# Optimization experiments

Measured on AMD Instinct MI355X. Metric: run time of the kernel, lower is better.

Reference implementation:

```python
import jax, jax.numpy as jnp
import numpy as np

# ---- dimensions ----
N = 16384      # nodes
E = 131072     # edges (avg degree 8)
F = 128        # scalar channel width == s_dim
L = 9          # spherical-harmonic components (lmax=2)
R = 8          # radial basis size
DOUT = L * F   # post-product node width (1152)
K = 1024       # fixed number of master nodes (static stand-in for m>0.5)
HID = 64       # master-selection hidden dim
DA = 64        # virtual-attention head dim
LAMBDA_ATTN = 0.5
R_CUT = 5.0
EPS = 1e-9


def sh_l2(u):
    # real SH polynomials up to l=2 on unit vectors u[..., 3] -> [..., 9]
    x, y, z = u[..., 0], u[..., 1], u[..., 2]
    o = jnp.ones_like(x)
    return jnp.stack([o, x, y, z, x * y, y * z, 3.0 * z * z - 1.0, x * z, x * x - y * y], axis=-1)


def bessel(r):
    # Bessel radial basis; r [..., 1] -> [..., R]
    n = jnp.arange(1, R + 1, dtype=r.dtype)
    return jnp.sqrt(2.0 / R_CUT) * jnp.sin(n * jnp.pi * r / R_CUT) / jnp.maximum(r, EPS)


def setup_inputs() -> dict:
    key = jax.random.key(0)
    ks = jax.random.split(key, 18)
    s = lambda d: 1.0 / np.sqrt(d)
    return {
        'h': jax.random.normal(ks[0], (N, F), jnp.float32),
        'pos': 3.0 * jax.random.normal(ks[1], (N, 3), jnp.float32),
        'edge_sh': jax.random.normal(ks[2], (E, L), jnp.float32),
        'edge_feats': jax.random.uniform(ks[3], (E, R), jnp.float32),
        'W_node_l': s(F) * jax.random.normal(ks[4], (F, F), jnp.float32),
        'W_rad_l': s(R) * jax.random.normal(ks[5], (R, F), jnp.float32),
        'W_prod_l': s(L * F) * jax.random.normal(ks[6], (L, F, DOUT), jnp.float32),
        'ms_W1': s(F) * jax.random.normal(ks[7], (F, HID), jnp.float32),
        'ms_b1': jnp.zeros((HID,), jnp.float32),
        'ms_W2': s(HID) * jax.random.normal(ks[8], (HID, 1), jnp.float32),
        'ms_b2': jnp.zeros((1,), jnp.float32),
        'vg_Wq': s(F) * jax.random.normal(ks[9], (F, DA), jnp.float32),
        'vg_Wk': s(F) * jax.random.normal(ks[10], (F, DA), jnp.float32),
        'W_node_h': s(DOUT) * jax.random.normal(ks[11], (DOUT, F), jnp.float32),
        'W_rad_h': s(R) * jax.random.normal(ks[12], (R, F), jnp.float32),
        'W_prod_h': s(L * F) * jax.random.normal(ks[13], (L, F, DOUT), jnp.float32),
        'edge_index': jax.random.randint(ks[14], (2, E), 0, N),
    }


def reference(h, pos, edge_sh, edge_feats, W_node_l, W_rad_l, W_prod_l,
              ms_W1, ms_b1, ms_W2, ms_b2, vg_Wq, vg_Wk,
              W_node_h, W_rad_h, W_prod_h, edge_index):
    src, dst = edge_index[0], edge_index[1]

    # ---- local conv + reshape + prod (with padded residual sc) ----
    t = (h[src] @ W_node_l) * (edge_feats @ W_rad_l)                      # [E,F]
    msg = edge_sh[:, :, None] * t[:, None, :]                             # [E,L,F]
    upd = jax.ops.segment_sum(msg, dst, num_segments=N)                   # [N,L,F]
    sc = jnp.pad(h, ((0, 0), (0, DOUT - F)))
    h_local = jnp.einsum('nlf,lfg->ng', upd, W_prod_l) + sc               # [N,DOUT]

    # ---- master selection (MLP -> sigmoid); fixed top-K masters ----
    hs = h_local[:, :F]
    m = jax.nn.sigmoid(jax.nn.relu(hs @ ms_W1 + ms_b1) @ ms_W2 + ms_b2)[:, 0]  # [N]
    _, midx = jax.lax.top_k(m, K)
    master_idx = jnp.sort(midx)                                           # [K]

    # ---- induced subgraph among masters as dense [K,K] adjacency ----
    rank = jnp.full((N,), K, dtype=jnp.int32).at[master_idx].set(jnp.arange(K, dtype=jnp.int32))
    adj = jnp.zeros((K + 1, K + 1), h.dtype).at[rank[src], rank[dst]].max(jnp.ones((E,), h.dtype))
    adj_induced = adj[:K, :K]

    h_m = h_local[master_idx]                                             # [K,DOUT]
    pos_m = pos[master_idx]                                               # [K,3]
    hms = h_m[:, :F]

    # ---- virtual graph generation (attention -> thresholded dense adj) ----
    q = hms @ vg_Wq
    kk = hms @ vg_Wk
    A = jax.nn.sigmoid(q @ kk.T / jnp.sqrt(jnp.asarray(DA, h.dtype)))     # [K,K]
    A_virtual = jnp.where(A > LAMBDA_ATTN, A, 0.0)
    eye = jnp.eye(K, dtype=bool)
    Bv = (A_virtual > 0) & ~eye                                           # remove self loops
    Bv = Bv | Bv.T                                                        # to_undirected
    adj_master = jnp.clip(adj_induced + Bv.astype(h.dtype), 0.0, 1.0) * (1.0 - jnp.eye(K, dtype=h.dtype))

    # ---- hierarchical conv over dense master graph ----
    A_rec = adj_master.T                                                  # A_rec[i,j]=1: sender j -> receiver i
    V = pos_m[None, :, :] - pos_m[:, None, :]                             # vec = pos[src]-pos[dst]
    r = jnp.linalg.norm(V, axis=-1, keepdims=True)                        # [K,K,1]
    u = V / jnp.maximum(r, EPS)
    sh_m = sh_l2(u)                                                       # [K,K,L]
    rad = bessel(r)                                                       # [K,K,R]
    tm = (h_m @ W_node_h)[None, :, :] * (rad @ W_rad_h) * A_rec[:, :, None]  # [K,K,F]
    upd_m = jnp.einsum('ijl,ijf->ilf', sh_m, tm)                          # [K,L,F]
    h_hier = jnp.einsum('ilf,lfg->ig', upd_m, W_prod_h) + h_m             # sc_master pad is 0-width

    # ---- masked scatter blend ----
    h_exp = jnp.zeros_like(h_local).at[master_idx].set(h_hier)
    h_final = (1.0 - m[:, None]) * h_local + m[:, None] * h_exp
    return (h_final, A_virtual, m, master_idx)
```

## Files before the change

### kernel.cpp

```cpp
#include <hip/hip_runtime.h>
#include <hip/hip_bf16.h>
#include <stdint.h>

#define N_NODES 16384
#define E_EDGES 131072
#define F_DIM 128
#define L_DIM 9
#define R_DIM 8
#define DOUT_DIM 1152
#define K_SEL 1024
#define HID_DIM 64
#define DA_DIM 64

typedef unsigned short u16;
typedef __attribute__((ext_vector_type(8))) short bf16x8;
typedef __attribute__((ext_vector_type(4))) float f32x4;

static __device__ inline u16 f2bs(float x) {
  union { __hip_bfloat16 b; u16 s; } u;
  u.b = __float2bfloat16(x);
  return u.s;
}

#define GLDS16(gsrc, ldst) __builtin_amdgcn_global_load_lds( \
    (__attribute__((address_space(1))) void*)(void*)(gsrc),  \
    (__attribute__((address_space(3))) void*)(ldst), 16, 0, 0)

__global__ __launch_bounds__(256) void gemm_mfma(
    const float* __restrict__ A, const u16* __restrict__ Bt,
    float* __restrict__ C, int ldc, int M, int Nc, int Kc,
    const float* __restrict__ Add, int ldadd, int addW)
{
  __shared__ float Af[128 * 32];
  __shared__ u16  Bs[128 * 32];
  const int tid = threadIdx.x;
  const int wave = tid >> 6, lane = tid & 63;
  const int wm = wave >> 1, wn = wave & 1;
  const int l15 = lane & 15, quad = lane >> 4;
  const int bm = blockIdx.y * 128, bn = blockIdx.x * 128;

  f32x4 acc[4][4];
#pragma unroll
  for (int i = 0; i < 4; i++)
#pragma unroll
    for (int j = 0; j < 4; j++) acc[i][j] = (f32x4)(0.f);

  for (int k0 = 0; k0 < Kc; k0 += 32) {
    __syncthreads();
#pragma unroll
    for (int it = 0; it < 4; it++) {
      int c = it * 256 + tid;
      int row = c >> 3, op = c & 7;
      int oct = op ^ (row & 7);
      const float* g = A + (size_t)(bm + row) * Kc + k0 + oct * 4;
      GLDS16(g, &Af[c * 4]);
    }
#pragma unroll
    for (int it = 0; it < 2; it++) {
      int c = it * 256 + tid;
      int row = c >> 2, qp = c & 3;
      int q = qp ^ ((row >> 1) & 3);
      const u16* g = Bt + (size_t)(bn + row) * Kc + k0 + q * 8;
      GLDS16(g, &Bs[c * 8]);
    }
    __syncthreads();

    bf16x8 af[4], bfg[4];
#pragma unroll
    for (int mi = 0; mi < 4; mi++) {
      int m = wm * 64 + mi * 16 + l15;
      int o0 = (quad * 2) ^ (m & 7), o1 = (quad * 2 + 1) ^ (m & 7);
      float4 lo = *(const float4*)&Af[m * 32 + o0 * 4];
      float4 hi = *(const float4*)&Af[m * 32 + o1 * 4];
      bf16x8 r;
      r[0] = (short)f2bs(lo.x); r[1] = (short)f2bs(lo.y);
      r[2] = (short)f2bs(lo.z); r[3] = (short)f2bs(lo.w);
      r[4] = (short)f2bs(hi.x); r[5] = (short)f2bs(hi.y);
      r[6] = (short)f2bs(hi.z); r[7] = (short)f2bs(hi.w);
      af[mi] = r;
    }
#pragma unroll
    for (int ni = 0; ni < 4; ni++) {
      int n = wn * 64 + ni * 16 + l15;
      int q2 = quad ^ ((n >> 1) & 3);
      bfg[ni] = *(const bf16x8*)&Bs[n * 32 + q2 * 8];
    }
#pragma unroll
    for (int mi = 0; mi < 4; mi++)
#pragma unroll
      for (int ni = 0; ni < 4; ni++)
        acc[mi][ni] = __builtin_amdgcn_mfma_f32_16x16x32_bf16(af[mi], bfg[ni], acc[mi][ni], 0, 0, 0);
  }
#pragma unroll
  for (int mi = 0; mi < 4; mi++)
#pragma unroll
    for (int ni = 0; ni < 4; ni++)
#pragma unroll
      for (int r = 0; r < 4; r++) {
        int row = bm + wm * 64 + mi * 16 + quad * 4 + r;
        int col = bn + wn * 64 + ni * 16 + l15;
        float v = acc[mi][ni][r];
        if (Add != nullptr && col < addW) v += Add[(size_t)row * ldadd + col];
        C[(size_t)row * ldc + col] = v;
      }
}

__global__ __launch_bounds__(256) void gemm_mfma_b16(
    const u16* __restrict__ A, const u16* __restrict__ Bt,
    float* __restrict__ C, int ldc, int Kc, int nbx, int nwg,
    const float* __restrict__ Add, int ldadd, int addW)
{
  __shared__ u16 As[2][128 * 32];
  __shared__ u16 Bs[2][128 * 32];
  const int tid = threadIdx.x;
  const int wave = tid >> 6, lane = tid & 63;
  const int wm = wave >> 1, wn = wave & 1;
  const int l15 = lane & 15, quad = lane >> 4;
  const int lin = blockIdx.x;
  const int swz = (lin & 7) * (nwg >> 3) + (lin >> 3);
  const int bm = (swz / nbx) * 128, bn = (swz % nbx) * 128;

  const int c0 = tid,      r0 = c0 >> 2, q0 = (c0 & 3) ^ ((r0 >> 1) & 3);
  const int c1 = 256 + tid, r1 = c1 >> 2, q1 = (c1 & 3) ^ ((r1 >> 1) & 3);
  const u16* gA0 = A + (size_t)(bm + r0) * Kc + q0 * 8;
  const u16* gA1 = A + (size_t)(bm + r1) * Kc + q1 * 8;
  const u16* gB0 = Bt + (size_t)(bn + r0) * Kc + q0 * 8;
  const u16* gB1 = Bt + (size_t)(bn + r1) * Kc + q1 * 8;

  f32x4 acc[4][4];
#pragma unroll
  for (int i = 0; i < 4; i++)
#pragma unroll
    for (int j = 0; j < 4; j++) acc[i][j] = (f32x4)(0.f);

#define STAGE_AB(s, k0) do {                      \
    GLDS16(gA0 + (k0), &As[s][c0 * 8]);           \
    GLDS16(gA1 + (k0), &As[s][c1 * 8]);           \
    GLDS16(gB0 + (k0), &Bs[s][c0 * 8]);           \
    GLDS16(gB1 + (k0), &Bs[s][c1 * 8]);           \
  } while (0)
#define RAWBAR() do { __builtin_amdgcn_s_barrier(); \
    __builtin_amdgcn_sched_barrier(0); } while (0)

  STAGE_AB(0, 0);
  asm volatile("s_waitcnt vmcnt(0)" ::: "memory");
  RAWBAR();
  int cur = 0;
  const int nt = Kc / 32;
  for (int t = 0; t < nt; t++) {
    if (t + 1 < nt) {
      STAGE_AB(cur ^ 1, (t + 1) * 32);
      asm volatile("s_waitcnt vmcnt(4)" ::: "memory");
    } else {
      asm volatile("s_waitcnt vmcnt(0)" ::: "memory");
    }
    RAWBAR();
    bf16x8 af[4], bfg[4];
#pragma unroll
    for (int mi = 0; mi < 4; mi++) {
      int m = wm * 64 + mi * 16 + l15;
      af[mi] = *(const bf16x8*)&As[cur][m * 32 + (quad ^ ((m >> 1) & 3)) * 8];
    }
#pragma unroll
    for (int ni = 0; ni < 4; ni++) {
      int n = wn * 64 + ni * 16 + l15;
      bfg[ni] = *(const bf16x8*)&Bs[cur][n * 32 + (quad ^ ((n >> 1) & 3)) * 8];
    }
#pragma unroll
    for (int mi = 0; mi < 4; mi++)
#pragma unroll
      for (int ni = 0; ni < 4; ni++)
        acc[mi][ni] = __builtin_amdgcn_mfma_f32_16x16x32_bf16(af[mi], bfg[ni], acc[mi][ni], 0, 0, 0);
    RAWBAR();
    cur ^= 1;
  }
#undef STAGE_AB
#undef RAWBAR

#pragma unroll
  for (int mi = 0; mi < 4; mi++)
#pragma unroll
    for (int ni = 0; ni < 4; ni++)
#pragma unroll
      for (int r = 0; r < 4; r++) {
        int row = bm + wm * 64 + mi * 16 + quad * 4 + r;
        int col = bn + wn * 64 + ni * 16 + l15;
        float v = acc[mi][ni][r];
        if (Add != nullptr && col < addW) v += Add[(size_t)row * ldadd + col];
        C[(size_t)row * ldc + col] = v;
      }
}

__global__ __launch_bounds__(256) void transpose_bf16(
    const float* __restrict__ W, u16* __restrict__ Bt, int K, int N)
{
  __shared__ float t[32][33];
  const int n0 = blockIdx.x * 32, k0 = blockIdx.y * 32;
  const int tx = threadIdx.x & 31, ty = threadIdx.x >> 5;
  for (int r = ty; r < 32; r += 8) t[r][tx] = W[(size_t)(k0 + r) * N + n0 + tx];
  __syncthreads();
  for (int r = ty; r < 32; r += 8) Bt[(size_t)(n0 + r) * K + k0 + tx] = f2bs(t[tx][r]);
}

__global__ __launch_bounds__(256) void hs_gemm_kernel(
    const float* __restrict__ A,
    const float* __restrict__ B,
    float* __restrict__ psum)
{
  __shared__ float As[16][129];
  __shared__ float Bs[16][128];
  const int tid = threadIdx.x;
  const int tx = tid & 15, ty = tid >> 4;
  const int bm = blockIdx.x * 128;
  const int z = blockIdx.y;
  const int kb = z * (DOUT_DIM / 4);
  const int ke = kb + DOUT_DIM / 4;
  const int ac = tid & 15, ar0 = tid >> 4;
  const int bc = tid & 127, br0 = tid >> 7;
  float acc[8][8];
#pragma unroll
  for (int i = 0; i < 8; i++)
#pragma unroll
    for (int j = 0; j < 8; j++) acc[i][j] = 0.f;

  float ra[8], rb[8];
#define LOADREG(k0) do {                                                       \
    _Pragma("unroll")                                                          \
    for (int rr = 0; rr < 8; rr++)                                             \
      ra[rr] = A[(size_t)(bm + ar0 + rr * 16) * DOUT_DIM + (k0) + ac];         \
    _Pragma("unroll")                                                          \
    for (int rr = 0; rr < 8; rr++)                                             \
      rb[rr] = B[(size_t)((k0) + br0 + rr * 2) * DOUT_DIM + bc];               \
  } while (0)

  LOADREG(kb);
  for (int k0 = kb; k0 < ke; k0 += 16) {
#pragma unroll
    for (int rr = 0; rr < 8; rr++) As[ac][ar0 + rr * 16] = ra[rr];
#pragma unroll
    for (int rr = 0; rr < 8; rr++) Bs[br0 + rr * 2][bc] = rb[rr];
    __syncthreads();
    if (k0 + 16 < ke) LOADREG(k0 + 16);
#pragma unroll
    for (int kk = 0; kk < 16; kk++) {
      float a[8], b[8];
#pragma unroll
      for (int i = 0; i < 8; i++) a[i] = As[kk][ty * 8 + i];
#pragma unroll
      for (int j = 0; j < 8; j++) b[j] = Bs[kk][tx * 8 + j];
#pragma unroll
      for (int i = 0; i < 8; i++)
#pragma unroll
        for (int j = 0; j < 8; j++) acc[i][j] = fmaf(a[i], b[j], acc[i][j]);
    }
    __syncthreads();
  }
#undef LOADREG
#pragma unroll
  for (int i = 0; i < 8; i++) {
    size_t row = (size_t)z * N_NODES + bm + ty * 8 + i;
#pragma unroll
    for (int j = 0; j < 8; j++)
      psum[row * F_DIM + tx * 8 + j] = acc[i][j];
  }
}

__global__ __launch_bounds__(256) void hs_reduce_kernel(
    const float* __restrict__ psum, const float* __restrict__ h, float* __restrict__ hs)
{
  size_t i4 = (size_t)blockIdx.x * 256 + threadIdx.x;
  const size_t stride = (size_t)N_NODES * F_DIM / 4;
  const float4* p = (const float4*)psum;
  float4 a = p[i4], b = p[i4 + stride], c = p[i4 + 2 * stride], d = p[i4 + 3 * stride];
  float4 hh = ((const float4*)h)[i4];
  float4 o;
  o.x = a.x + b.x + c.x + d.x + hh.x;
  o.y = a.y + b.y + c.y + d.y + hh.y;
  o.z = a.z + b.z + c.z + d.z + hh.z;
  o.w = a.w + b.w + c.w + d.w + hh.w;
  ((float4*)hs)[i4] = o;
}

__global__ __launch_bounds__(256) void gemm64_f32(
    const float* __restrict__ A, int lda,
    const float* __restrict__ B, int ldb,
    float* __restrict__ C, int ldc,
    int M, int Nc, int Kc, int kPerSplit,
    const float* __restrict__ Add, int ldadd, int addW)
{
  __shared__ float As[16][65];
  __shared__ float Bs[16][64];
  const int tid = threadIdx.x;
  const int tx = tid & 15, ty = tid >> 4;
  const int bm = blockIdx.y * 64, bn = blockIdx.x * 64;
  const int kb = blockIdx.z * kPerSplit;
  const int ke = min(kb + kPerSplit, Kc);
  float acc[4][4];
#pragma unroll
  for (int i = 0; i < 4; i++)
#pragma unroll
    for (int j = 0; j < 4; j++) acc[i][j] = 0.f;
  for (int k0 = kb; k0 < ke; k0 += 16) {
    const int ac = tid & 15, ar = tid >> 4;
#pragma unroll
    for (int rr = 0; rr < 4; rr++) {
      int row = ar + rr * 16;
      As[ac][row] = A[(size_t)(bm + row) * lda + k0 + ac];
    }
    const int bc = tid & 63, br = tid >> 6;
#pragma unroll
    for (int rr = 0; rr < 4; rr++) {
      int kr = br + rr * 4;
      Bs[kr][bc] = B[(size_t)(k0 + kr) * ldb + bn + bc];
    }
    __syncthreads();
#pragma unroll
    for (int kk = 0; kk < 16; kk++) {
      float a[4], b[4];
#pragma unroll
      for (int i = 0; i < 4; i++) a[i] = As[kk][ty * 4 + i];
#pragma unroll
      for (int j = 0; j < 4; j++) b[j] = Bs[kk][tx * 4 + j];
#pragma unroll
      for (int i = 0; i < 4; i++)
#pragma unroll
        for (int j = 0; j < 4; j++) acc[i][j] = fmaf(a[i], b[j], acc[i][j]);
    }
    __syncthreads();
  }
#pragma unroll
  for (int i = 0; i < 4; i++) {
    int row = bm + ty * 4 + i;
#pragma unroll
    for (int j = 0; j < 4; j++) {
      int col = bn + tx * 4 + j;
      if (gridDim.z > 1) {
        atomicAdd(&C[(size_t)row * ldc + col], acc[i][j]);
      } else {
        float v = acc[i][j];
        if (Add != nullptr && col < addW) v += Add[(size_t)row * ldadd + col];
        C[(size_t)row * ldc + col] = v;
      }
    }
  }
}

__global__ __launch_bounds__(256) void count_kernel(
    const int* __restrict__ ei, int* __restrict__ counts)
{
  int e = blockIdx.x * 256 + threadIdx.x;
  atomicAdd(&counts[ei[E_EDGES + e]], 1);
}

__global__ __launch_bounds__(1024) void scan_kernel(
    const int* __restrict__ counts, int* __restrict__ offsets, int* __restrict__ cursor)
{
  __shared__ int part[1024];
  const int t = threadIdx.x;
  const int base = t * 16;
  int loc[16];
  int s = 0;
#pragma unroll
  for (int k = 0; k < 16; k++) { loc[k] = counts[base + k]; s += loc[k]; }
  part[t] = s;
  __syncthreads();
  for (int d = 1; d < 1024; d <<= 1) {
    int v = (t >= d) ? part[t - d] : 0;
    __syncthreads();
    part[t] += v;
    __syncthreads();
  }
  int run = part[t] - s;
#pragma unroll
  for (int k = 0; k < 16; k++) {
    offsets[base + k] = run;
    cursor[base + k] = run;
    run += loc[k];
  }
}

__global__ __launch_bounds__(256) void fill_kernel(
    const int* __restrict__ ei, int* __restrict__ cursor, int* __restrict__ elist)
{
  int e = blockIdx.x * 256 + threadIdx.x;
  int d = ei[E_EDGES + e];
  int p = atomicAdd(&cursor[d], 1);
  elist[p] = e;
}

__global__ __launch_bounds__(128) void gather_accum_kernel(
    const float* __restrict__ hW, const float* __restrict__ edge_sh,
    const float* __restrict__ edge_feats, const float* __restrict__ W_rad_l,
    const int* __restrict__ ei, const int* __restrict__ offsets,
    const int* __restrict__ counts, const int* __restrict__ elist,
    float* __restrict__ upd, u16* __restrict__ updb)
{
  const int d = blockIdx.x, f = threadIdx.x;
  const float w0 = W_rad_l[0 * F_DIM + f], w1 = W_rad_l[1 * F_DIM + f];
  const float w2 = W_rad_l[2 * F_DIM + f], w3 = W_rad_l[3 * F_DIM + f];
  const float w4 = W_rad_l[4 * F_DIM + f], w5 = W_rad_l[5 * F_DIM + f];
  const float w6 = W_rad_l[6 * F_DIM + f], w7 = W_rad_l[7 * F_DIM + f];
  const int b = offsets[d], n = counts[d];
  float acc[L_DIM];
#pragma unroll
  for (int l = 0; l < L_DIM; l++) acc[l] = 0.f;
  for (int k = 0; k < n; k++) {
    const int e = elist[b + k];
    const int s = ei[e];
    const float4 ef0 = *(const float4*)&edge_feats[(size_t)e * R_DIM];
    const float4 ef1 = *(const float4*)&edge_feats[(size_t)e * R_DIM + 4];
    float rw = ef0.x * w0;
    rw = fmaf(ef0.y, w1, rw); rw = fmaf(ef0.z, w2, rw); rw = fmaf(ef0.w, w3, rw);
    rw = fmaf(ef1.x, w4, rw); rw = fmaf(ef1.y, w5, rw);
    rw = fmaf(ef1.z, w6, rw); rw = fmaf(ef1.w, w7, rw);
    const float tf = hW[(size_t)s * F_DIM + f] * rw;
#pragma unroll
    for (int l = 0; l < L_DIM; l++)
      acc[l] = fmaf(edge_sh[(size_t)e * L_DIM + l], tf, acc[l]);
  }
#pragma unroll
  for (int l = 0; l < L_DIM; l++)
    upd[(size_t)d * DOUT_DIM + l * F_DIM + f] = acc[l];
  if (updb != nullptr) {
#pragma unroll
    for (int l = 0; l < L_DIM; l++)
      updb[(size_t)d * DOUT_DIM + l * F_DIM + f] = f2bs(acc[l]);
  }
}

__global__ __launch_bounds__(256) void gate_kernel(
    const float* __restrict__ hs, const float* __restrict__ W1,
    const float* __restrict__ b1, const float* __restrict__ W2,
    const float* __restrict__ b2, float* __restrict__ m_ws, float* __restrict__ m_out,
    int* __restrict__ hist1)
{
  __shared__ float sW1[F_DIM * HID_DIM];
  __shared__ float srow[4][F_DIM];
  const int tid = threadIdx.x;
  for (int t = tid; t < F_DIM * HID_DIM; t += 256) sW1[t] = W1[t];
  const int wave = tid >> 6, lane = tid & 63;
  const int n = blockIdx.x * 4 + wave;
  srow[wave][lane] = hs[(size_t)n * F_DIM + lane];
  srow[wave][lane + 64] = hs[(size_t)n * F_DIM + lane + 64];
  __syncthreads();
  float hid = b1[lane];
#pragma unroll 8
  for (int c = 0; c < F_DIM; c++) hid = fmaf(srow[wave][c], sW1[c * HID_DIM + lane], hid);
  hid = fmaxf(hid, 0.f);
  float v = hid * W2[lane];
#pragma unroll
  for (int off = 32; off > 0; off >>= 1) v += __shfl_down(v, off);
  if (lane == 0) {
    float mm = 1.f / (1.f + expf(-(v + b2[0])));
    m_ws[n] = mm;
    m_out[n] = mm;
    unsigned mb = __float_as_uint(mm);
    atomicAdd(&hist1[mb >> 16], 1);
  }
}

__global__ __launch_bounds__(1024) void radix_sel_kernel(
    const int* __restrict__ hist, const int* __restrict__ kin, int kinIdx,
    int* __restrict__ outp, int outIdx)
{
  __shared__ int part[1024];
  const int t = threadIdx.x;
  const int Kv = kin ? kin[kinIdx] : K_SEL;
  const int base = t * 64;
  int s = 0;
  for (int k = 0; k < 64; k++) s += hist[base + k];
  part[t] = s;
  __syncthreads();
  for (int d = 1; d < 1024; d <<= 1) {
    int v = (t + d < 1024) ? part[t + d] : 0;
    __syncthreads();
    part[t] += v;
    __syncthreads();
  }
  int inc = part[t];
  if (inc >= Kv && inc - s < Kv) {
    int r = inc - s;
    for (int b = base + 63; b >= base; b--) {
      int hv = hist[b];
      if (r + hv >= Kv) { outp[outIdx] = b; outp[outIdx + 1] = Kv - r; break; }
      r += hv;
    }
  }
}

__global__ __launch_bounds__(256) void hist2_kernel(
    const float* __restrict__ m_ws, const int* __restrict__ selb, int* __restrict__ hist2)
{
  int i = blockIdx.x * 256 + threadIdx.x;
  unsigned mb = __float_as_uint(m_ws[i]);
  if ((int)(mb >> 16) == selb[0]) atomicAdd(&hist2[mb & 0xFFFFu], 1);
}

__global__ __launch_bounds__(256) void flag_kernel(
    const float* __restrict__ m_ws, int* __restrict__ selb,
    unsigned char* __restrict__ flags, int* __restrict__ cand)
{
  int i = blockIdx.x * 256 + threadIdx.x;
  unsigned mb = __float_as_uint(m_ws[i]);
  unsigned vb = ((unsigned)selb[0] << 16) | (unsigned)selb[2];
  unsigned char fl = 0;
  if (mb > vb) fl = 1;
  else if (mb == vb) { int p = atomicAdd(&selb[4], 1); cand[p] = i; }
  flags[i] = fl;
}

__global__ __launch_bounds__(1024) void cand_kernel(
    const int* __restrict__ selb, const int* __restrict__ cand, unsigned char* __restrict__ flags)
{
  const int nc = selb[4], need = selb[3];
  for (int c = threadIdx.x; c < nc; c += 1024) {
    const int idx = cand[c];
    int r = 0;
    for (int o = 0; o < nc; o++) r += (cand[o] < idx) ? 1 : 0;
    if (r < need) flags[idx] = 1;
  }
}

__global__ __launch_bounds__(1024) void compact_kernel(
    const unsigned char* __restrict__ flags, int* __restrict__ midx,
    int* __restrict__ rank, float* __restrict__ mi_out)
{
  __shared__ int part[1024];
  const int t = threadIdx.x;
  const int base = t * 16;
  int loc[16];
  int s = 0;
#pragma unroll
  for (int k = 0; k < 16; k++) { loc[k] = flags[base + k]; s += loc[k]; }
  part[t] = s;
  __syncthreads();
  for (int d = 1; d < 1024; d <<= 1) {
    int v = (t >= d) ? part[t - d] : 0;
    __syncthreads();
    part[t] += v;
    __syncthreads();
  }
  int run = part[t] - s;
#pragma unroll
  for (int k = 0; k < 16; k++) {
    int i = base + k;
    if (loc[k]) {
      midx[run] = i;
      mi_out[run] = (float)i;
      rank[i] = run;
      run++;
    } else {
      rank[i] = K_SEL;
    }
  }
}

__global__ __launch_bounds__(256) void adj_kernel(
    const int* __restrict__ ei, const int* __restrict__ rank,
    unsigned char* __restrict__ adjm, unsigned char* __restrict__ adjT)
{
  int e = blockIdx.x * 256 + threadIdx.x;
  int rs = rank[ei[e]];
  int rd = rank[ei[E_EDGES + e]];
  if (rs < K_SEL && rd < K_SEL) {
    adjm[(size_t)rs * K_SEL + rd] = 1;
    adjT[(size_t)rd * K_SEL + rs] = 1;
  }
}

__global__ __launch_bounds__(128) void gather_kernel(
    const float* __restrict__ hl, const float* __restrict__ pos,
    const int* __restrict__ midx, float* __restrict__ h_m, float* __restrict__ pos_m)
{
  const int rI = blockIdx.x, t = threadIdx.x;
  const int mi = midx[rI];
  const float4* src = (const float4*)(hl + (size_t)mi * DOUT_DIM);
  float4* dst = (float4*)(h_m + (size_t)rI * DOUT_DIM);
  for (int c = t; c < DOUT_DIM / 4; c += 128) dst[c] = src[c];
  if (t < 3) pos_m[rI * 3 + t] = pos[mi * 3 + t];
}

__global__ __launch_bounds__(128) void qk_kernel(
    const float* __restrict__ hs, const int* __restrict__ midx,
    const float* __restrict__ Wq, const float* __restrict__ Wk,
    float* __restrict__ q, float* __restrict__ kk)
{
  __shared__ float row[F_DIM];
  const int i = blockIdx.x, t = threadIdx.x;
  const int mi = midx[i];
  row[t] = hs[(size_t)mi * F_DIM + t];
  __syncthreads();
  const int d = t & 63;
  const float* W = (t < 64) ? Wq : Wk;
  float acc = 0.f;
#pragma unroll 8
  for (int c = 0; c < F_DIM; c++) acc = fmaf(row[c], W[c * DA_DIM + d], acc);
  float* dst = (t < 64) ? q : kk;
  dst[(size_t)i * DA_DIM + d] = acc;
}

__global__ __launch_bounds__(256) void attn_kernel(
    const float* __restrict__ q, const float* __restrict__ kk,
    unsigned char* __restrict__ maskA, unsigned char* __restrict__ maskAT,
    float* __restrict__ Av)
{
  __shared__ float qs[16][DA_DIM + 1], ks[16][DA_DIM + 1];
  const int tx = threadIdx.x, ty = threadIdx.y;
  const int tid = ty * 16 + tx;
  const int i0 = blockIdx.y * 16, j0 = blockIdx.x * 16;
  for (int t = tid; t < 16 * DA_DIM; t += 256) {
    int rr = t >> 6, cc = t & 63;
    qs[rr][cc] = q[(size_t)(i0 + rr) * DA_DIM + cc];
    ks[rr][cc] = kk[(size_t)(j0 + rr) * DA_DIM + cc];
  }
  __syncthreads();
  float acc = 0.f;
#pragma unroll
  for (int d2 = 0; d2 < DA_DIM; d2++) acc = fmaf(qs[ty][d2], ks[tx][d2], acc);
  float sgl = 1.f / (1.f + expf(-acc * 0.125f));
  size_t o = (size_t)(i0 + ty) * K_SEL + (j0 + tx);
  bool big = sgl > 0.5f;
  unsigned char bb = big ? 1 : 0;
  maskA[o] = bb;
  maskAT[(size_t)(j0 + tx) * K_SEL + (i0 + ty)] = bb;
  Av[o] = big ? sgl : 0.f;
}

__global__ __launch_bounds__(256) void listbuild_kernel(
    const unsigned char* __restrict__ adjT, const unsigned char* __restrict__ maskAT,
    const unsigned char* __restrict__ maskA, u16* __restrict__ list, int* __restrict__ nj)
{
  __shared__ int cnt;
  const int i = blockIdx.x, tid = threadIdx.x;
  const int lane = tid & 63;
  if (tid == 0) cnt = 0;
  __syncthreads();
  const int j0 = tid * 4;
  uchar4 a  = *(const uchar4*)&adjT  [(size_t)i * K_SEL + j0];
  uchar4 mt = *(const uchar4*)&maskAT[(size_t)i * K_SEL + j0];
  uchar4 ma = *(const uchar4*)&maskA [(size_t)i * K_SEL + j0];
  unsigned char av[4];
  av[0] = a.x | mt.x | ma.x; av[1] = a.y | mt.y | ma.y;
  av[2] = a.z | mt.z | ma.z; av[3] = a.w | mt.w | ma.w;
#pragma unroll
  for (int r = 0; r < 4; r++) {
    int j = j0 + r;
    bool e = (j != i) && av[r];
    unsigned long long m = __ballot(e);
    int nset = __popcll(m);
    int base = 0;
    if (lane == 0 && nset) base = atomicAdd(&cnt, nset);
    base = __shfl(base, 0);
    if (e) {
      int p = base + __popcll(m & ((1ull << lane) - 1ull));
      list[(size_t)i * K_SEL + p] = (u16)j;
    }
  }
  __syncthreads();
  if (tid == 0) nj[i] = cnt;
}

__global__ __launch_bounds__(512) void hier2_kernel(
    const float* __restrict__ hWn, const float* __restrict__ pos_m,
    const float* __restrict__ W_rad_h, const u16* __restrict__ list,
    const int* __restrict__ nj, float* __restrict__ upd_m, u16* __restrict__ updb_m)
{
  __shared__ float gsm[128][20];
  __shared__ float red[3][L_DIM][F_DIM];
  const int tid = threadIdx.x;
  const int i = blockIdx.x;
  const int f = tid & 127, jsub = tid >> 7;
  const float sw0 = W_rad_h[0 * F_DIM + f], sw1 = W_rad_h[1 * F_DIM + f];
  const float sw2 = W_rad_h[2 * F_DIM + f], sw3 = W_rad_h[3 * F_DIM + f];
  const float sw4 = W_rad_h[4 * F_DIM + f], sw5 = W_rad_h[5 * F_DIM + f];
  const float sw6 = W_rad_h[6 * F_DIM + f], sw7 = W_rad_h[7 * F_DIM + f];
  const float pix = pos_m[i * 3 + 0], piy = pos_m[i * 3 + 1], piz = pos_m[i * 3 + 2];
  float acc[L_DIM];
#pragma unroll
  for (int l = 0; l < L_DIM; l++) acc[l] = 0.f;
  const int n = nj[i];
  for (int c0 = 0; c0 < n; c0 += 128) {
    const int cnt = min(128, n - c0);
    __syncthreads();
    if (tid < cnt) {
      const int j = list[(size_t)i * K_SEL + c0 + tid];
      float vx = pos_m[j * 3 + 0] - pix;
      float vy = pos_m[j * 3 + 1] - piy;
      float vz = pos_m[j * 3 + 2] - piz;
      float r = sqrtf(vx * vx + vy * vy + vz * vz);
      float rm = fmaxf(r, 1e-9f);
      float inv = 1.f / rm;
      float ux = vx * inv, uy = vy * inv, uz = vz * inv;
      float theta = 0.62831853071795864769f * r;
      float s1 = sinf(theta), c1 = cosf(theta);
      float coef = 0.632455532033675866f * inv;
      float snm2 = 0.f, snm1 = s1;
      gsm[tid][0] = s1 * coef;
#pragma unroll
      for (int nn = 2; nn <= R_DIM; nn++) {
        float sn = 2.f * c1 * snm1 - snm2;
        gsm[tid][nn - 1] = sn * coef;
        snm2 = snm1; snm1 = sn;
      }
      gsm[tid][8] = 1.f; gsm[tid][9] = ux; gsm[tid][10] = uy; gsm[tid][11] = uz;
      gsm[tid][12] = ux * uy; gsm[tid][13] = uy * uz;
      gsm[tid][14] = 3.f * uz * uz - 1.f;
      gsm[tid][15] = ux * uz; gsm[tid][16] = ux * ux - uy * uy;
      gsm[tid][17] = __int_as_float(j);
      gsm[tid][18] = 0.f; gsm[tid][19] = 0.f;
    }
    __syncthreads();
    for (int t = jsub; t < cnt; t += 4) {
      float2 s2 = *(const float2*)&gsm[t][16];
      const int j = __float_as_int(s2.y);
      const float hw = hWn[(size_t)j * F_DIM + f];
      float4 r0 = *(const float4*)&gsm[t][0];
      float4 r1 = *(const float4*)&gsm[t][4];
      float4 s0 = *(const float4*)&gsm[t][8];
      float4 s1g = *(const float4*)&gsm[t][12];
      float rw = r0.x * sw0;
      rw = fmaf(r0.y, sw1, rw); rw = fmaf(r0.z, sw2, rw); rw = fmaf(r0.w, sw3, rw);
      rw = fmaf(r1.x, sw4, rw); rw = fmaf(r1.y, sw5, rw);
      rw = fmaf(r1.z, sw6, rw); rw = fmaf(r1.w, sw7, rw);
      const float tm = hw * rw;
      acc[0] = fmaf(s0.x, tm, acc[0]); acc[1] = fmaf(s0.y, tm, acc[1]);
      acc[2] = fmaf(s0.z, tm, acc[2]); acc[3] = fmaf(s0.w, tm, acc[3]);
      acc[4] = fmaf(s1g.x, tm, acc[4]); acc[5] = fmaf(s1g.y, tm, acc[5]);
      acc[6] = fmaf(s1g.z, tm, acc[6]); acc[7] = fmaf(s1g.w, tm, acc[7]);
      acc[8] = fmaf(s2.x, tm, acc[8]);
    }
  }
  __syncthreads();
  if (jsub > 0) {
#pragma unroll
    for (int l = 0; l < L_DIM; l++) red[jsub - 1][l][f] = acc[l];
  }
  __syncthreads();
  if (jsub == 0) {
#pragma unroll
    for (int l = 0; l < L_DIM; l++) {
      float v = acc[l] + red[0][l][f] + red[1][l][f] + red[2][l][f];
      upd_m[(size_t)i * DOUT_DIM + l * F_DIM + f] = v;
      updb_m[(size_t)i * DOUT_DIM + l * F_DIM + f] = f2bs(v);
    }
  }
}

__global__ __launch_bounds__(256) void combine_kernel(
    float* __restrict__ out0, const float* __restrict__ h_hier,
    const float* __restrict__ m_ws, const int* __restrict__ rank)
{
  size_t i4 = (size_t)blockIdx.x * 256 + threadIdx.x;
  int n = (int)(i4 / (DOUT_DIM / 4));
  int g4 = (int)(i4 % (DOUT_DIM / 4));
  float mv = m_ws[n];
  int r = rank[n];
  float4 hl = ((const float4*)out0)[i4];
  float4 he = make_float4(0.f, 0.f, 0.f, 0.f);
  if (r < K_SEL) he = ((const float4*)h_hier)[(size_t)r * (DOUT_DIM / 4) + g4];
  float4 o;
  o.x = (1.f - mv) * hl.x + mv * he.x;
  o.y = (1.f - mv) * hl.y + mv * he.y;
  o.z = (1.f - mv) * hl.z + mv * he.z;
  o.w = (1.f - mv) * hl.w + mv * he.w;
  ((float4*)out0)[i4] = o;
}

extern "C" void kernel_launch(void* const* d_in, const int* in_sizes, int n_in,
                              void* d_out, int out_size, void* d_ws, size_t ws_size,
                              hipStream_t stream)
{
  const float* h         = (const float*)d_in[0];
  const float* pos       = (const float*)d_in[1];
  const float* edge_sh   = (const float*)d_in[2];
  const float* edge_feats= (const float*)d_in[3];
  const float* W_node_l  = (const float*)d_in[4];
  const float* W_rad_l   = (const float*)d_in[5];
  const float* W_prod_l  = (const float*)d_in[6];
  const float* ms_W1     = (const float*)d_in[7];
  const float* ms_b1     = (const float*)d_in[8];
  const float* ms_W2     = (const float*)d_in[9];
  const float* ms_b2     = (const float*)d_in[10];
  const float* vg_Wq     = (const float*)d_in[11];
  const float* vg_Wk     = (const float*)d_in[12];
  const float* W_node_h  = (const float*)d_in[13];
  const float* W_rad_h   = (const float*)d_in[14];
  const float* W_prod_h  = (const float*)d_in[15];
  const int*   eidx      = (const int*)d_in[16];

  float* out    = (float*)d_out;
  float* out_hf = out;
  float* out_Av = out + (size_t)N_NODES * DOUT_DIM;
  float* out_m  = out_Av + (size_t)K_SEL * K_SEL;
  float* out_mi = out_m + N_NODES;

  char* ws = (char*)d_ws;
  float* upd = (float*)ws;
  float* hW  = (float*)(ws + (size_t)N_NODES * DOUT_DIM * 4);
  float* hs  = hW;
  const size_t updbOff = (size_t)N_NODES * DOUT_DIM * 4 + (size_t)N_NODES * F_DIM * 4;
  const size_t updbNeed = updbOff + (size_t)N_NODES * DOUT_DIM * 2;
  const bool useB16 = (ws_size >= updbNeed);
  u16* updb = (u16*)(ws + updbOff);
  float* psum = out_hf;
  u16* Btl = (u16*)out_Av;
  char* csr = (char*)out_Av + (((size_t)DOUT_DIM * DOUT_DIM * 2 + 255) & ~(size_t)255);
  int* counts  = (int*)csr;
  int* offsets = counts + N_NODES;
  int* cursor  = offsets + N_NODES;
  int* elist   = cursor + N_NODES;
  size_t off = 0;
  auto alloc = [&](size_t bytes) -> void* {
    void* p = ws + off;
    off += (bytes + 255) & ~(size_t)255;
    return p;
  };
  float* m_ws  = (float*)alloc((size_t)N_NODES * 4);
  int*   rank  = (int*)alloc((size_t)N_NODES * 4);
  int*   midx  = (int*)alloc((size_t)K_SEL * 4);
  int*   hist1 = (int*)alloc((size_t)65536 * 4);
  int*   hist2 = (int*)alloc((size_t)65536 * 4);
  int*   selb  = (int*)alloc((size_t)64 * 4);
  int*   cand  = (int*)alloc((size_t)N_NODES * 4);
  unsigned char* flags = (unsigned char*)alloc((size_t)N_NODES);
  unsigned char* adjm  = (unsigned char*)alloc((size_t)K_SEL * K_SEL);
  unsigned char* adjT  = (unsigned char*)alloc((size_t)K_SEL * K_SEL);
  unsigned char* maskA = (unsigned char*)alloc((size_t)K_SEL * K_SEL);
  unsigned char* maskAT= (unsigned char*)alloc((size_t)K_SEL * K_SEL);
  float* qbuf  = (float*)alloc((size_t)K_SEL * DA_DIM * 4);
  float* kbuf  = (float*)alloc((size_t)K_SEL * DA_DIM * 4);
  float* h_m   = (float*)alloc((size_t)K_SEL * DOUT_DIM * 4);
  float* pos_m = (float*)alloc((size_t)K_SEL * 3 * 4);
  float* hWn   = (float*)alloc((size_t)K_SEL * F_DIM * 4);
  float* upd_m = (float*)alloc((size_t)K_SEL * DOUT_DIM * 4);
  float* h_hier= (float*)alloc((size_t)K_SEL * DOUT_DIM * 4);
  u16*   Bth   = (u16*)alloc((size_t)DOUT_DIM * DOUT_DIM * 2);
  u16*   jlist = (u16*)alloc((size_t)K_SEL * K_SEL * 2);
  int*   njbuf = (int*)alloc((size_t)K_SEL * 4);
  u16*   updbm = (u16*)alloc((size_t)K_SEL * DOUT_DIM * 2);

  hipMemsetAsync(counts, 0, (size_t)N_NODES * 4, stream);
  transpose_bf16<<<dim3(DOUT_DIM / 32, DOUT_DIM / 32), 256, 0, stream>>>(
      W_prod_l, Btl, DOUT_DIM, DOUT_DIM);
  gemm64_f32<<<dim3(F_DIM / 64, N_NODES / 64, 1), 256, 0, stream>>>(
      h, F_DIM, W_node_l, F_DIM, hW, F_DIM, N_NODES, F_DIM, F_DIM, F_DIM, nullptr, 0, 0);
  count_kernel<<<E_EDGES / 256, 256, 0, stream>>>(eidx, counts);
  scan_kernel<<<1, 1024, 0, stream>>>(counts, offsets, cursor);
  fill_kernel<<<E_EDGES / 256, 256, 0, stream>>>(eidx, cursor, elist);
  gather_accum_kernel<<<N_NODES, 128, 0, stream>>>(
      hW, edge_sh, edge_feats, W_rad_l, eidx, offsets, counts, elist, upd,
      useB16 ? updb : nullptr);
  hs_gemm_kernel<<<dim3(N_NODES / 128, 4), 256, 0, stream>>>(upd, W_prod_l, psum);
  hs_reduce_kernel<<<(N_NODES * F_DIM / 4) / 256, 256, 0, stream>>>(psum, h, hs);
  if (useB16) {
    gemm_mfma_b16<<<(DOUT_DIM / 128) * (N_NODES / 128), 256, 0, stream>>>(
        updb, Btl, out_hf, DOUT_DIM, DOUT_DIM, DOUT_DIM / 128,
        (DOUT_DIM / 128) * (N_NODES / 128), h, F_DIM, F_DIM);
  } else {
    gemm_mfma<<<dim3(DOUT_DIM / 128, N_NODES / 128), 256, 0, stream>>>(
        upd, Btl, out_hf, DOUT_DIM, N_NODES, DOUT_DIM, DOUT_DIM, h, F_DIM, F_DIM);
  }

  hipMemsetAsync(adjm, 0, (size_t)2 * K_SEL * K_SEL, stream);
  hipMemsetAsync(hist1, 0, (size_t)65536 * 4 * 2 + 256, stream);
  transpose_bf16<<<dim3(DOUT_DIM / 32, DOUT_DIM / 32), 256, 0, stream>>>(
      W_prod_h, Bth, DOUT_DIM, DOUT_DIM);
  gate_kernel<<<N_NODES / 4, 256, 0, stream>>>(hs, ms_W1, ms_b1, ms_W2, ms_b2,
                                               m_ws, out_m, hist1);
  radix_sel_kernel<<<1, 1024, 0, stream>>>(hist1, nullptr, 0, selb, 0);
  hist2_kernel<<<N_NODES / 256, 256, 0, stream>>>(m_ws, selb, hist2);
  radix_sel_kernel<<<1, 1024, 0, stream>>>(hist2, selb, 1, selb, 2);
  flag_kernel<<<N_NODES / 256, 256, 0, stream>>>(m_ws, selb, flags, cand);
  cand_kernel<<<1, 1024, 0, stream>>>(selb, cand, flags);
  compact_kernel<<<1, 1024, 0, stream>>>(flags, midx, rank, out_mi);
  adj_kernel<<<E_EDGES / 256, 256, 0, stream>>>(eidx, rank, adjm, adjT);
  gather_kernel<<<K_SEL, 128, 0, stream>>>(out_hf, pos, midx, h_m, pos_m);
  qk_kernel<<<K_SEL, 128, 0, stream>>>(hs, midx, vg_Wq, vg_Wk, qbuf, kbuf);
  attn_kernel<<<dim3(K_SEL / 16, K_SEL / 16), dim3(16, 16), 0, stream>>>(
      qbuf, kbuf, maskA, maskAT, out_Av);
  listbuild_kernel<<<K_SEL, 256, 0, stream>>>(adjT, maskAT, maskA, jlist, njbuf);
  hipMemsetAsync(hWn, 0, (size_t)K_SEL * F_DIM * 4, stream);
  gemm64_f32<<<dim3(F_DIM / 64, K_SEL / 64, 4), 256, 0, stream>>>(
      h_m, DOUT_DIM, W_node_h, F_DIM, hWn, F_DIM,
      K_SEL, F_DIM, DOUT_DIM, DOUT_DIM / 4, nullptr, 0, 0);
  hier2_kernel<<<K_SEL, 512, 0, stream>>>(hWn, pos_m, W_rad_h, jlist, njbuf, upd_m, updbm);
  gemm_mfma_b16<<<(DOUT_DIM / 128) * (K_SEL / 128), 256, 0, stream>>>(
      updbm, Bth, h_hier, DOUT_DIM, DOUT_DIM, DOUT_DIM / 128,
      (DOUT_DIM / 128) * (K_SEL / 128), h_m, DOUT_DIM, DOUT_DIM);
  combine_kernel<<<(N_NODES * DOUT_DIM / 4) / 256, 256, 0, stream>>>(out_hf, h_hier, m_ws, rank);
}
```

Measured before the change: 667.8 us.

## Fuse candidate tie-break into compaction, retile hier2 kernel, simplify GEMM barriers

Merges the candidate tie-break kernel into the compaction kernel, saving one single-block launch. The hier2 kernel is remapped to 256 threads that each handle two feature channels, and it no longer writes the unused fp32 upd_m buffer, only the bf16 copy. The bf16 MFMA GEMM drops its hand-placed vmcnt waits and scheduling barriers in favour of one __syncthreads per K step. This relies on __syncthreads also waiting for the async LDS loads. The barrier change can reduce load/compute overlap, and halving threads in hier2 lowers occupancy while raising per-thread work.

```diff
diff --git a/kernel.cpp b/kernel.cpp
--- a/kernel.cpp
+++ b/kernel.cpp
@@ -139,22 +139,13 @@
     GLDS16(gB0 + (k0), &Bs[s][c0 * 8]);           \
     GLDS16(gB1 + (k0), &Bs[s][c1 * 8]);           \
   } while (0)
-#define RAWBAR() do { __builtin_amdgcn_s_barrier(); \
-    __builtin_amdgcn_sched_barrier(0); } while (0)
 
   STAGE_AB(0, 0);
-  asm volatile("s_waitcnt vmcnt(0)" ::: "memory");
-  RAWBAR();
+  __syncthreads();
   int cur = 0;
   const int nt = Kc / 32;
   for (int t = 0; t < nt; t++) {
-    if (t + 1 < nt) {
-      STAGE_AB(cur ^ 1, (t + 1) * 32);
-      asm volatile("s_waitcnt vmcnt(4)" ::: "memory");
-    } else {
-      asm volatile("s_waitcnt vmcnt(0)" ::: "memory");
-    }
-    RAWBAR();
+    if (t + 1 < nt) STAGE_AB(cur ^ 1, (t + 1) * 32);
     bf16x8 af[4], bfg[4];
 #pragma unroll
     for (int mi = 0; mi < 4; mi++) {
@@ -171,11 +162,10 @@
 #pragma unroll
       for (int ni = 0; ni < 4; ni++)
         acc[mi][ni] = __builtin_amdgcn_mfma_f32_16x16x32_bf16(af[mi], bfg[ni], acc[mi][ni], 0, 0, 0);
-    RAWBAR();
+    __syncthreads();
     cur ^= 1;
   }
 #undef STAGE_AB
-#undef RAWBAR
 
 #pragma unroll
   for (int mi = 0; mi < 4; mi++)
@@ -509,24 +499,21 @@
   flags[i] = fl;
 }
 
-__global__ __launch_bounds__(1024) void cand_kernel(
-    const int* __restrict__ selb, const int* __restrict__ cand, unsigned char* __restrict__ flags)
-{
+__global__ __launch_bounds__(1024) void compact_kernel(
+    const int* __restrict__ selb, const int* __restrict__ cand,
+    unsigned char* flags, int* __restrict__ midx,
+    int* __restrict__ rank, float* __restrict__ mi_out)
+{
+  __shared__ int part[1024];
+  const int t = threadIdx.x;
   const int nc = selb[4], need = selb[3];
-  for (int c = threadIdx.x; c < nc; c += 1024) {
+  for (int c = t; c < nc; c += 1024) {
     const int idx = cand[c];
     int r = 0;
     for (int o = 0; o < nc; o++) r += (cand[o] < idx) ? 1 : 0;
     if (r < need) flags[idx] = 1;
   }
-}
-
-__global__ __launch_bounds__(1024) void compact_kernel(
-    const unsigned char* __restrict__ flags, int* __restrict__ midx,
-    int* __restrict__ rank, float* __restrict__ mi_out)
-{
-  __shared__ int part[1024];
-  const int t = threadIdx.x;
+  __syncthreads();
   const int base = t * 16;
   int loc[16];
   int s = 0;
@@ -660,24 +647,29 @@
   if (tid == 0) nj[i] = cnt;
 }
 
-__global__ __launch_bounds__(512) void hier2_kernel(
+__global__ __launch_bounds__(256) void hier2_kernel(
     const float* __restrict__ hWn, const float* __restrict__ pos_m,
     const float* __restrict__ W_rad_h, const u16* __restrict__ list,
-    const int* __restrict__ nj, float* __restrict__ upd_m, u16* __restrict__ updb_m)
+    const int* __restrict__ nj, u16* __restrict__ updb_m)
 {
   __shared__ float gsm[128][20];
   __shared__ float red[3][L_DIM][F_DIM];
   const int tid = threadIdx.x;
   const int i = blockIdx.x;
-  const int f = tid & 127, jsub = tid >> 7;
-  const float sw0 = W_rad_h[0 * F_DIM + f], sw1 = W_rad_h[1 * F_DIM + f];
-  const float sw2 = W_rad_h[2 * F_DIM + f], sw3 = W_rad_h[3 * F_DIM + f];
-  const float sw4 = W_rad_h[4 * F_DIM + f], sw5 = W_rad_h[5 * F_DIM + f];
-  const float sw6 = W_rad_h[6 * F_DIM + f], sw7 = W_rad_h[7 * F_DIM + f];
+  const int lane = tid & 63, jsub = tid >> 6;
+  const int f0 = lane, f1 = lane + 64;
+  const float a0 = W_rad_h[0 * F_DIM + f0], a1 = W_rad_h[1 * F_DIM + f0];
+  const float a2 = W_rad_h[2 * F_DIM + f0], a3 = W_rad_h[3 * F_DIM + f0];
+  const float a4 = W_rad_h[4 * F_DIM + f0], a5 = W_rad_h[5 * F_DIM + f0];
+  const float a6 = W_rad_h[6 * F_DIM + f0], a7 = W_rad_h[7 * F_DIM + f0];
+  const float b0 = W_rad_h[0 * F_DIM + f1], b1 = W_rad_h[1 * F_DIM + f1];
+  const float b2 = W_rad_h[2 * F_DIM + f1], b3 = W_rad_h[3 * F_DIM + f1];
+  const float b4 = W_rad_h[4 * F_DIM + f1], b5 = W_rad_h[5 * F_DIM + f1];
+  const float b6 = W_rad_h[6 * F_DIM + f1], b7 = W_rad_h[7 * F_DIM + f1];
   const float pix = pos_m[i * 3 + 0], piy = pos_m[i * 3 + 1], piz = pos_m[i * 3 + 2];
-  float acc[L_DIM];
-#pragma unroll
-  for (int l = 0; l < L_DIM; l++) acc[l] = 0.f;
+  float acc0[L_DIM], acc1[L_DIM];
+#pragma unroll
+  for (int l = 0; l < L_DIM; l++) { acc0[l] = 0.f; acc1[l] = 0.f; }
   const int n = nj[i];
   for (int c0 = 0; c0 < n; c0 += 128) {
     const int cnt = min(128, n - c0);
@@ -713,35 +705,49 @@
     for (int t = jsub; t < cnt; t += 4) {
       float2 s2 = *(const float2*)&gsm[t][16];
       const int j = __float_as_int(s2.y);
-      const float hw = hWn[(size_t)j * F_DIM + f];
+      const float hw0 = hWn[(size_t)j * F_DIM + f0];
+      const float hw1 = hWn[(size_t)j * F_DIM + f1];
       float4 r0 = *(const float4*)&gsm[t][0];
       float4 r1 = *(const float4*)&gsm[t][4];
       float4 s0 = *(const float4*)&gsm[t][8];
       float4 s1g = *(const float4*)&gsm[t][12];
-      float rw = r0.x * sw0;
-      rw = fmaf(r0.y, sw1, rw); rw = fmaf(r0.z, sw2, rw); rw = fmaf(r0.w, sw3, rw);
-      rw = fmaf(r1.x, sw4, rw); rw = fmaf(r1.y, sw5, rw);
-      rw = fmaf(r1.z, sw6, rw); rw = fmaf(r1.w, sw7, rw);
-      const float tm = hw * rw;
-      acc[0] = fmaf(s0.x, tm, acc[0]); acc[1] = fmaf(s0.y, tm, acc[1]);
-      acc[2] = fmaf(s0.z, tm, acc[2]); acc[3] = fmaf(s0.w, tm, acc[3]);
-      acc[4] = fmaf(s1g.x, tm, acc[4]); acc[5] = fmaf(s1g.y, tm, acc[5]);
-      acc[6] = fmaf(s1g.z, tm, acc[6]); acc[7] = fmaf(s1g.w, tm, acc[7]);
-      acc[8] = fmaf(s2.x, tm, acc[8]);
+      float rwa = r0.x * a0;
+      rwa = fmaf(r0.y, a1, rwa); rwa = fmaf(r0.z, a2, rwa); rwa = fmaf(r0.w, a3, rwa);
+      rwa = fmaf(r1.x, a4, rwa); rwa = fmaf(r1.y, a5, rwa);
+      rwa = fmaf(r1.z, a6, rwa); rwa = fmaf(r1.w, a7, rwa);
+      float rwb = r0.x * b0;
+      rwb = fmaf(r0.y, b1, rwb); rwb = fmaf(r0.z, b2, rwb); rwb = fmaf(r0.w, b3, rwb);
+      rwb = fmaf(r1.x, b4, rwb); rwb = fmaf(r1.y, b5, rwb);
+      rwb = fmaf(r1.z, b6, rwb); rwb = fmaf(r1.w, b7, rwb);
+      const float tm0 = hw0 * rwa;
+      const float tm1 = hw1 * rwb;
+      acc0[0] = fmaf(s0.x, tm0, acc0[0]); acc1[0] = fmaf(s0.x, tm1, acc1[0]);
+      acc0[1] = fmaf(s0.y, tm0, acc0[1]); acc1[1] = fmaf(s0.y, tm1, acc1[1]);
+      acc0[2] = fmaf(s0.z, tm0, acc0[2]); acc1[2] = fmaf(s0.z, tm1, acc1[2]);
+      acc0[3] = fmaf(s0.w, tm0, acc0[3]); acc1[3] = fmaf(s0.w, tm1, acc1[3]);
+      acc0[4] = fmaf(s1g.x, tm0, acc0[4]); acc1[4] = fmaf(s1g.x, tm1, acc1[4]);
+      acc0[5] = fmaf(s1g.y, tm0, acc0[5]); acc1[5] = fmaf(s1g.y, tm1, acc1[5]);
+      acc0[6] = fmaf(s1g.z, tm0, acc0[6]); acc1[6] = fmaf(s1g.z, tm1, acc1[6]);
+      acc0[7] = fmaf(s1g.w, tm0, acc0[7]); acc1[7] = fmaf(s1g.w, tm1, acc1[7]);
+      acc0[8] = fmaf(s2.x, tm0, acc0[8]); acc1[8] = fmaf(s2.x, tm1, acc1[8]);
     }
   }
   __syncthreads();
   if (jsub > 0) {
 #pragma unroll
-    for (int l = 0; l < L_DIM; l++) red[jsub - 1][l][f] = acc[l];
+    for (int l = 0; l < L_DIM; l++) {
+      red[jsub - 1][l][f0] = acc0[l];
+      red[jsub - 1][l][f1] = acc1[l];
+    }
   }
   __syncthreads();
   if (jsub == 0) {
 #pragma unroll
     for (int l = 0; l < L_DIM; l++) {
-      float v = acc[l] + red[0][l][f] + red[1][l][f] + red[2][l][f];
-      upd_m[(size_t)i * DOUT_DIM + l * F_DIM + f] = v;
-      updb_m[(size_t)i * DOUT_DIM + l * F_DIM + f] = f2bs(v);
+      float v0 = acc0[l] + red[0][l][f0] + red[1][l][f0] + red[2][l][f0];
+      float v1 = acc1[l] + red[0][l][f1] + red[1][l][f1] + red[2][l][f1];
+      updb_m[(size_t)i * DOUT_DIM + l * F_DIM + f0] = f2bs(v0);
+      updb_m[(size_t)i * DOUT_DIM + l * F_DIM + f1] = f2bs(v1);
     }
   }
 }
@@ -838,6 +844,7 @@
   u16*   jlist = (u16*)alloc((size_t)K_SEL * K_SEL * 2);
   int*   njbuf = (int*)alloc((size_t)K_SEL * 4);
   u16*   updbm = (u16*)alloc((size_t)K_SEL * DOUT_DIM * 2);
+  (void)upd_m;
 
   hipMemsetAsync(counts, 0, (size_t)N_NODES * 4, stream);
   transpose_bf16<<<dim3(DOUT_DIM / 32, DOUT_DIM / 32), 256, 0, stream>>>(
@@ -871,8 +878,7 @@
   hist2_kernel<<<N_NODES / 256, 256, 0, stream>>>(m_ws, selb, hist2);
   radix_sel_kernel<<<1, 1024, 0, stream>>>(hist2, selb, 1, selb, 2);
   flag_kernel<<<N_NODES / 256, 256, 0, stream>>>(m_ws, selb, flags, cand);
-  cand_kernel<<<1, 1024, 0, stream>>>(selb, cand, flags);
-  compact_kernel<<<1, 1024, 0, stream>>>(flags, midx, rank, out_mi);
+  compact_kernel<<<1, 1024, 0, stream>>>(selb, cand, flags, midx, rank, out_mi);
   adj_kernel<<<E_EDGES / 256, 256, 0, stream>>>(eidx, rank, adjm, adjT);
   gather_kernel<<<K_SEL, 128, 0, stream>>>(out_hf, pos, midx, h_m, pos_m);
   qk_kernel<<<K_SEL, 128, 0, stream>>>(hs, midx, vg_Wq, vg_Wk, qbuf, kbuf);
@@ -883,7 +889,7 @@
   gemm64_f32<<<dim3(F_DIM / 64, K_SEL / 64, 4), 256, 0, stream>>>(
       h_m, DOUT_DIM, W_node_h, F_DIM, hWn, F_DIM,
       K_SEL, F_DIM, DOUT_DIM, DOUT_DIM / 4, nullptr, 0, 0);
-  hier2_kernel<<<K_SEL, 512, 0, stream>>>(hWn, pos_m, W_rad_h, jlist, njbuf, upd_m, updbm);
+  hier2_kernel<<<K_SEL, 256, 0, stream>>>(hWn, pos_m, W_rad_h, jlist, njbuf, updbm);
   gemm_mfma_b16<<<(DOUT_DIM / 128) * (K_SEL / 128), 256, 0, stream>>>(
       updbm, Bth, h_hier, DOUT_DIM, DOUT_DIM, DOUT_DIM / 128,
       (DOUT_DIM / 128) * (K_SEL / 128), h_m, DOUT_DIM, DOUT_DIM);
```

Result: faster. 649.2 us (-2.8%).
